# Kernel optimization log

Measured on AMD Instinct MI355X. Metric: run time of the kernel, lower is better.

Reference implementation:

```python
import jax, jax.numpy as jnp
import numpy as np

N_E = 8192
E_DIM = 64
BETA = 0.25


def setup_inputs() -> dict:
    key = jax.random.key(0)
    k_z, k_e = jax.random.split(key)
    z = jax.random.normal(k_z, (16, E_DIM, 64, 64), dtype=jnp.float32)  # b c h w
    # nn.Embedding weight init: uniform(-1/n_e, 1/n_e)
    embedding = jax.random.uniform(
        k_e, (N_E, E_DIM), dtype=jnp.float32, minval=-1.0 / N_E, maxval=1.0 / N_E
    )
    return {"z": z, "embedding": embedding}


def reference(z, embedding):
    # b c h w -> b h w c
    zc = jnp.transpose(z, (0, 2, 3, 1))
    zf = zc.reshape(-1, embedding.shape[1])  # [N, d]
    # squared euclidean distances: ||z||^2 + ||e||^2 - 2 z.e
    d = (
        jnp.sum(zf * zf, axis=1, keepdims=True)
        + jnp.sum(embedding * embedding, axis=1)
        - 2.0 * jnp.einsum("nd,kd->nk", zf, embedding)
    )  # [N, K]
    min_encoding_indices = jnp.argmin(d, axis=1)  # [N]
    z_q = jnp.take(embedding, min_encoding_indices, axis=0).reshape(zc.shape)
    # legacy=True loss
    loss = jnp.mean((jax.lax.stop_gradient(z_q) - zc) ** 2) + BETA * jnp.mean(
        (z_q - jax.lax.stop_gradient(zc)) ** 2
    )
    # straight-through estimator
    z_q = zc + jax.lax.stop_gradient(z_q - zc)
    z_q = jnp.transpose(z_q, (0, 3, 1, 2))  # b h w c -> b c h w
    return z_q, loss, min_encoding_indices
```

## Files before the change

kernel.cpp:

```cpp
#include <hip/hip_runtime.h>

#define NTOT 65536
#define KC   8192
#define DV   64
#define ZQN  4194304
#define NSPL 4
#define KSL  2048
#define NTILE 16
#define CAP2 16
#define SLA  44u
#define SLE  40u

typedef unsigned int u32;
typedef unsigned long long u64;
typedef unsigned short ushort;
typedef short short8 __attribute__((ext_vector_type(8)));
typedef float float4v __attribute__((ext_vector_type(4)));

__device__ __forceinline__ short f2bf(float x) {
    u32 u = __float_as_uint(x);
    u32 r = (u + 0x7fffu + ((u >> 16) & 1u)) >> 16;
    return (short)r;
}

__device__ __forceinline__ float exact_d(float A, float B,
                                         const float* __restrict__ zr,
                                         const float* __restrict__ e) {
#pragma clang fp contract(off)
    float u0 = 0.f, u1 = 0.f, u2 = 0.f, u3 = 0.f;
#pragma unroll
    for (int i = 0; i < 4; ++i) {
        const int t = 16 * i;
        u0 = (zr[t+0]*e[t+0]) + ((zr[t+4]*e[t+4]) + ((zr[t+8]*e[t+8]) + ((zr[t+12]*e[t+12]) + u0)));
        u1 = (zr[t+1]*e[t+1]) + ((zr[t+5]*e[t+5]) + ((zr[t+9]*e[t+9]) + ((zr[t+13]*e[t+13]) + u1)));
        u2 = (zr[t+2]*e[t+2]) + ((zr[t+6]*e[t+6]) + ((zr[t+10]*e[t+10]) + ((zr[t+14]*e[t+14]) + u2)));
        u3 = (zr[t+3]*e[t+3]) + ((zr[t+7]*e[t+7]) + ((zr[t+11]*e[t+11]) + ((zr[t+15]*e[t+15]) + u3)));
    }
    float dot = (u0 + u1) + (u2 + u3);
    return (A + B) - (2.0f * dot);
}

__global__ __launch_bounds__(256) void vq_prep(
    const float* __restrict__ emb, const float* __restrict__ z,
    float* __restrict__ nrm, float* __restrict__ An,
    u32* __restrict__ cnt, double* __restrict__ lacc,
    ushort* __restrict__ ebs) {
    const int tid = blockIdx.x * 256 + threadIdx.x;
    const int t = tid >> 10, r = tid & 1023;
    const int s = r >> 7, r2 = r & 127, h = r2 >> 6, l = r2 & 63;
    const int q = l >> 4, c = l & 15;
    const float* src = emb + (size_t)((t * 128 + s * 16 + c) * 64 + h * 32 + q * 8);
    short8 v;
#pragma unroll
    for (int j = 0; j < 8; ++j) v[j] = f2bf(src[j]);
    *reinterpret_cast<short8*>(ebs + (size_t)tid * 8) = v;
    cnt[tid] = 0u;
    {
        const float* zp = z + (size_t)(tid >> 12) * 262144 + (tid & 4095);
        double ad = 0.0;
#pragma unroll
        for (int d = 0; d < DV; ++d) {
            double x = (double)zp[(size_t)d * 4096];
            ad = fma(x, x, ad);
        }
        An[tid] = (float)ad;
    }
    if (tid < KC) {
        double sacc = 0.0;
#pragma unroll
        for (int d = 0; d < DV; ++d) {
            double x = (double)emb[(size_t)tid * DV + d];
            sacc = fma(x, x, sacc);
        }
        nrm[tid] = (float)sacc;
    }
    if (tid == 0) *lacc = 0.0;
}

__global__ __launch_bounds__(256)
void vq_pass(const float* __restrict__ z, const ushort* __restrict__ ebs,
             u32* __restrict__ cnt, u32* __restrict__ cand) {
    const int tid = threadIdx.x;
    const int lane = tid & 63;
    const int nblk = blockIdx.x & 255, ks = blockIdx.x >> 8;
    const int nb = nblk * 256 + (tid >> 6) * 64;
    const int col = lane & 15, quad = lane >> 4;
    const int nlo = nb + col;

    short8 zf[4][2];
#pragma unroll
    for (int ns = 0; ns < 4; ++ns) {
        int n = nlo + ns * 16;
        const float* zp = z + (size_t)(n >> 12) * 262144 + (n & 4095);
#pragma unroll
        for (int t2 = 0; t2 < 2; ++t2)
#pragma unroll
            for (int j = 0; j < 8; ++j)
                zf[ns][t2][j] = f2bf(zp[(size_t)(t2 * 32 + quad * 8 + j) * 4096]);
    }

    u32 r0[4] = {0, 0, 0, 0}, r1[4] = {0, 0, 0, 0}, r2[4] = {0, 0, 0, 0};
    const char* gs = (const char*)ebs + (size_t)ks * (KSL * DV * 2);

    for (int t = 0; t < NTILE; ++t) {
#pragma unroll
        for (int g2 = 0; g2 < 4; ++g2) {
            const char* tb = gs + t * 16384 + g2 * 4096;
            short8 a00 = *reinterpret_cast<const short8*>(tb + lane * 16);
            short8 a01 = *reinterpret_cast<const short8*>(tb + 1024 + lane * 16);
            short8 a10 = *reinterpret_cast<const short8*>(tb + 2048 + lane * 16);
            short8 a11 = *reinterpret_cast<const short8*>(tb + 3072 + lane * 16);
            const u32 lowc = 0x80000000u + (u32)(((t * 4 + g2) << 2) | quad);
#pragma unroll
            for (int ns = 0; ns < 4; ++ns) {
                float4v acc0 = {0.f, 0.f, 0.f, 0.f};
                float4v acc1 = {0.f, 0.f, 0.f, 0.f};
                acc0 = __builtin_amdgcn_mfma_f32_16x16x32_bf16(a00, zf[ns][0], acc0, 0, 0, 0);
                acc0 = __builtin_amdgcn_mfma_f32_16x16x32_bf16(a01, zf[ns][1], acc0, 0, 0, 0);
                acc1 = __builtin_amdgcn_mfma_f32_16x16x32_bf16(a10, zf[ns][0], acc1, 0, 0, 0);
                acc1 = __builtin_amdgcn_mfma_f32_16x16x32_bf16(a11, zf[ns][1], acc1, 0, 0, 0);
                float q0 = fmaxf(fmaxf(acc0[0], acc0[1]), acc0[2]);
                float q1 = fmaxf(fmaxf(acc0[3], acc1[0]), acc1[1]);
                float q2 = fmaxf(fmaxf(acc1[2], acc1[3]), q0);
                float m  = fmaxf(q2, q1);
                u32 e = ((u32)(int)(m * 1048576.0f) << 16) + lowc;
                u32 x  = min(r0[ns], e);
                r0[ns] = max(r0[ns], e);
                u32 y  = min(r1[ns], x);
                r1[ns] = max(r1[ns], x);
                r2[ns] = max(r2[ns], y);
            }
        }
    }

#pragma unroll
    for (int ns = 0; ns < 4; ++ns) {
        u32 m = r0[ns];
        m = max(m, __shfl_xor(m, 16));
        m = max(m, __shfl_xor(m, 32));
        const u32 thr = (m & 0xffff0000u) - (SLA << 16);
        const int n = nlo + ns * 16;
        const u32 tag = (u32)ks << 8;
        if (r0[ns] >= thr) {
            u32 p = atomicAdd(&cnt[n], 1u);
            if (p < CAP2) cand[(size_t)n * CAP2 + p] = r0[ns] | tag;
        }
        if (r1[ns] >= thr) {
            u32 p = atomicAdd(&cnt[n], 1u);
            if (p < CAP2) cand[(size_t)n * CAP2 + p] = r1[ns] | tag;
        }
        if (r2[ns] >= thr) {
            u32 p = atomicAdd(&cnt[n], 1u);
            if (p < CAP2) cand[(size_t)n * CAP2 + p] = r2[ns] | tag;
        }
    }
}

__global__ __launch_bounds__(256) void vq_e1f(
    const float* __restrict__ z, const float* __restrict__ emb,
    const float* __restrict__ nrm, const float* __restrict__ An,
    const u32* __restrict__ cnt, const u32* __restrict__ cand,
    int* __restrict__ idxw, float* __restrict__ out,
    double* __restrict__ lacc) {
    __shared__ float zs[64][40];
    __shared__ int skmin[32];
    __shared__ double red[4];
    const int tid = threadIdx.x;
    const int n0 = blockIdx.x * 32;
    const int b = n0 >> 12, hw0 = n0 & 4095;
    {
        const float* zb = z + (size_t)b * 262144 + hw0;
        const int dS = tid >> 3, i4 = (tid & 7) * 4;
#pragma unroll
        for (int j = 0; j < 2; ++j) {
            const int d = dS + 32 * j;
            float4 v = *reinterpret_cast<const float4*>(zb + (size_t)d * 4096 + i4);
            *reinterpret_cast<float4*>(&zs[d][i4]) = v;
        }
    }
    __syncthreads();

    const int li = tid >> 3;
    const int n = n0 + li;
    const int j8 = tid & 7;
    u32 c = min(cnt[n], (u32)CAP2);
    u32 emax = 0u;
    for (u32 j = 0; j < c; ++j) {
        u32 e = cand[(size_t)n * CAP2 + j];
        if (e > emax) emax = e;
    }
    const u32 ethr = (emax & 0xffff0000u) - (SLE << 16);

    float zr[DV];
#pragma unroll
    for (int d = 0; d < DV; ++d) zr[d] = zs[d][li];
    const float A = An[n];

    float dmin = 1e30f;
    int kmin = 0x7fffffff;
    const int st = j8 & 1;
    for (u32 j = (u32)(j8 >> 1); j < c; j += 4) {
        u32 e = cand[(size_t)n * CAP2 + j];
        if (e < ethr) continue;
        int s   = (int)(e >> 8) & 3;
        int grp = (int)(e >> 2) & 63;
        int q   = (int)e & 3;
        int base = s * KSL + grp * 32 + q * 4 + st * 16;
#pragma unroll
        for (int r = 0; r < 4; ++r) {
            int k = base + r;
            float d = exact_d(A, nrm[k], zr, emb + (size_t)k * DV);
            if (d < dmin || (d == dmin && k < kmin)) { dmin = d; kmin = k; }
        }
    }
    u64 key = ((u64)__float_as_uint(dmin) << 32) | (u32)kmin;
    u64 o1 = __shfl_xor(key, 1, 64); if (o1 < key) key = o1;
    u64 o2 = __shfl_xor(key, 2, 64); if (o2 < key) key = o2;
    u64 o4 = __shfl_xor(key, 4, 64); if (o4 < key) key = o4;
    if (j8 == 0) {
        int km = (int)(key & 0xffffffffu);
        idxw[n] = km;
        out[(size_t)ZQN + 1 + n] = (float)km;
        skmin[li] = km;
    }
    __syncthreads();

    const int nl = tid & 31, cg = tid >> 5;
    const int km2 = skmin[nl];
    const bool skipStore = (b >= 1 && b <= 4);
    const float4* er4 = (const float4*)(emb + (size_t)km2 * DV + cg * 8);
    float4 ev0 = er4[0], ev1 = er4[1];
    float vv[8] = {ev0.x, ev0.y, ev0.z, ev0.w, ev1.x, ev1.y, ev1.z, ev1.w};
    double lsum = 0.0;
#pragma unroll
    for (int u = 0; u < 8; ++u) {
        const int cc = cg * 8 + u;
        const float v = vv[u];
        if (!skipStore)
            out[(size_t)b * 262144 + (size_t)cc * 4096 + hw0 + nl] = v;
        double dv = (double)v - (double)zs[cc][nl];
        lsum = fma(dv, dv, lsum);
    }
#pragma unroll
    for (int off = 32; off > 0; off >>= 1)
        lsum += __shfl_down(lsum, off, 64);
    if ((tid & 63) == 0) red[tid >> 6] = lsum;
    __syncthreads();
    if (tid == 0)
        atomicAdd(lacc, red[0] + red[1] + red[2] + red[3]);
}

__global__ __launch_bounds__(256) void vq_bf(
    const float* __restrict__ emb, const int* __restrict__ idxw,
    const double* __restrict__ lacc, float* __restrict__ out) {
    const int gid = blockIdx.x * 256 + threadIdx.x;
    const int e0 = 262144 + gid * 4;
    const int b = e0 >> 18, rem = e0 & 262143;
    const int cc = rem >> 12, hw = rem & 4095;
    const int n = (b << 12) | hw;
    const int4 kk = *reinterpret_cast<const int4*>(idxw + n);
    float4 v;
    v.x = emb[(size_t)kk.x * DV + cc];
    v.y = emb[(size_t)kk.y * DV + cc];
    v.z = emb[(size_t)kk.z * DV + cc];
    v.w = emb[(size_t)kk.w * DV + cc];
    *reinterpret_cast<float4*>(out + e0) = v;
    if (gid == 0)
        out[ZQN] = (float)(1.25 * (*lacc) / (double)ZQN);
}

extern "C" void kernel_launch(void* const* d_in, const int* in_sizes, int n_in,
                              void* d_out, int out_size, void* d_ws, size_t ws_size,
                              hipStream_t stream) {
    const float* z   = (const float*)d_in[0];
    const float* emb = (const float*)d_in[1];
    float* out = (float*)d_out;

    ushort* ebs  = (ushort*)d_out;
    u32*    cand = (u32*)((char*)d_out + 1048576);
    double* lacc  = (double*)d_ws;
    float*  nrm   = (float*)((char*)d_ws + 64);
    u32*    cnt   = (u32*)((char*)d_ws + 32832);
    int*    idxw  = (int*)((char*)d_ws + 294976);
    float*  An    = (float*)((char*)d_ws + 819264);

    vq_prep<<<256, 256, 0, stream>>>(emb, z, nrm, An, cnt, lacc, ebs);
    vq_pass<<<NSPL * 256, 256, 0, stream>>>(z, ebs, cnt, cand);
    vq_e1f<<<2048, 256, 0, stream>>>(z, emb, nrm, An, cnt, cand, idxw, out, lacc);
    vq_bf<<<1024, 256, 0, stream>>>(emb, idxw, lacc, out);
}
```

Baseline: 246.4 us.

## Split exact rescoring from gather and loss, widen rescoring to 16 lanes per row

The exact-distance rescoring kernel now runs 512 threads per block with 16 lanes per row, each lane checking 2 codewords per candidate instead of 4. The gather, z_q store and loss reduction move into a separate kernel that handles all rows uniformly. That kernel computes the final loss with a last-block ticket counter, so the former final kernel is removed. The aim is more parallelism in the latency-bound rescoring step and a simpler store pattern. In exchange, z is re-read in the second kernel and there is an extra atomic ticket per block.

```diff
diff --git a/kernel.cpp b/kernel.cpp
--- a/kernel.cpp
+++ b/kernel.cpp
@@ -44,7 +44,7 @@
     const float* __restrict__ emb, const float* __restrict__ z,
     float* __restrict__ nrm, float* __restrict__ An,
     u32* __restrict__ cnt, double* __restrict__ lacc,
-    ushort* __restrict__ ebs) {
+    u32* __restrict__ ticket, ushort* __restrict__ ebs) {
     const int tid = blockIdx.x * 256 + threadIdx.x;
     const int t = tid >> 10, r = tid & 1023;
     const int s = r >> 7, r2 = r & 127, h = r2 >> 6, l = r2 & 63;
@@ -74,7 +74,7 @@
         }
         nrm[tid] = (float)sacc;
     }
-    if (tid == 0) *lacc = 0.0;
+    if (tid == 0) { *lacc = 0.0; *ticket = 0u; }
 }
 
 __global__ __launch_bounds__(256)
@@ -156,33 +156,27 @@
     }
 }
 
-__global__ __launch_bounds__(256) void vq_e1f(
+__global__ __launch_bounds__(512) void vq_e1(
     const float* __restrict__ z, const float* __restrict__ emb,
     const float* __restrict__ nrm, const float* __restrict__ An,
     const u32* __restrict__ cnt, const u32* __restrict__ cand,
-    int* __restrict__ idxw, float* __restrict__ out,
-    double* __restrict__ lacc) {
+    int* __restrict__ idxw, float* __restrict__ out) {
     __shared__ float zs[64][40];
-    __shared__ int skmin[32];
-    __shared__ double red[4];
     const int tid = threadIdx.x;
     const int n0 = blockIdx.x * 32;
     const int b = n0 >> 12, hw0 = n0 & 4095;
     {
         const float* zb = z + (size_t)b * 262144 + hw0;
         const int dS = tid >> 3, i4 = (tid & 7) * 4;
-#pragma unroll
-        for (int j = 0; j < 2; ++j) {
-            const int d = dS + 32 * j;
-            float4 v = *reinterpret_cast<const float4*>(zb + (size_t)d * 4096 + i4);
-            *reinterpret_cast<float4*>(&zs[d][i4]) = v;
-        }
+        float4 v = *reinterpret_cast<const float4*>(zb + (size_t)dS * 4096 + i4);
+        *reinterpret_cast<float4*>(&zs[dS][i4]) = v;
     }
     __syncthreads();
 
-    const int li = tid >> 3;
+    const int lane = tid & 63;
+    const int li = (tid >> 6) * 4 + (lane >> 4);
     const int n = n0 + li;
-    const int j8 = tid & 7;
+    const int j16 = lane & 15;
     u32 c = min(cnt[n], (u32)CAP2);
     u32 emax = 0u;
     for (u32 j = 0; j < c; ++j) {
@@ -198,16 +192,17 @@
 
     float dmin = 1e30f;
     int kmin = 0x7fffffff;
-    const int st = j8 & 1;
-    for (u32 j = (u32)(j8 >> 1); j < c; j += 4) {
+    const int st  = (j16 >> 1) & 1;
+    const int r0p = (j16 & 1) * 2;
+    for (u32 j = (u32)(j16 >> 2); j < c; j += 4) {
         u32 e = cand[(size_t)n * CAP2 + j];
         if (e < ethr) continue;
         int s   = (int)(e >> 8) & 3;
         int grp = (int)(e >> 2) & 63;
         int q   = (int)e & 3;
-        int base = s * KSL + grp * 32 + q * 4 + st * 16;
-#pragma unroll
-        for (int r = 0; r < 4; ++r) {
+        int base = s * KSL + grp * 32 + q * 4 + st * 16 + r0p;
+#pragma unroll
+        for (int r = 0; r < 2; ++r) {
             int k = base + r;
             float d = exact_d(A, nrm[k], zr, emb + (size_t)k * DV);
             if (d < dmin || (d == dmin && k < kmin)) { dmin = d; kmin = k; }
@@ -217,56 +212,53 @@
     u64 o1 = __shfl_xor(key, 1, 64); if (o1 < key) key = o1;
     u64 o2 = __shfl_xor(key, 2, 64); if (o2 < key) key = o2;
     u64 o4 = __shfl_xor(key, 4, 64); if (o4 < key) key = o4;
-    if (j8 == 0) {
+    u64 o8 = __shfl_xor(key, 8, 64); if (o8 < key) key = o8;
+    if (j16 == 0) {
         int km = (int)(key & 0xffffffffu);
         idxw[n] = km;
         out[(size_t)ZQN + 1 + n] = (float)km;
-        skmin[li] = km;
-    }
-    __syncthreads();
-
-    const int nl = tid & 31, cg = tid >> 5;
-    const int km2 = skmin[nl];
-    const bool skipStore = (b >= 1 && b <= 4);
-    const float4* er4 = (const float4*)(emb + (size_t)km2 * DV + cg * 8);
-    float4 ev0 = er4[0], ev1 = er4[1];
-    float vv[8] = {ev0.x, ev0.y, ev0.z, ev0.w, ev1.x, ev1.y, ev1.z, ev1.w};
+    }
+}
+
+__global__ __launch_bounds__(256) void vq_e2(
+    const float* __restrict__ z, const float* __restrict__ emb,
+    const int* __restrict__ idxw, float* __restrict__ out,
+    double* __restrict__ lacc, u32* __restrict__ ticket) {
+    __shared__ double red[4];
+    const int tid = threadIdx.x;
+    const int n = blockIdx.x * 64 + (tid & 63);
+    const int part = tid >> 6;
+    const int b = n >> 12, hw = n & 4095;
+    const int kmin = idxw[n];
+    const float* zp = z + (size_t)b * 262144 + hw;
+    const float4* er4 = (const float4*)(emb + (size_t)kmin * DV + part * 16);
     double lsum = 0.0;
 #pragma unroll
-    for (int u = 0; u < 8; ++u) {
-        const int cc = cg * 8 + u;
-        const float v = vv[u];
-        if (!skipStore)
-            out[(size_t)b * 262144 + (size_t)cc * 4096 + hw0 + nl] = v;
-        double dv = (double)v - (double)zs[cc][nl];
-        lsum = fma(dv, dv, lsum);
+    for (int i4 = 0; i4 < 4; ++i4) {
+        float4 ev = er4[i4];
+#pragma unroll
+        for (int u = 0; u < 4; ++u) {
+            int c = part * 16 + i4 * 4 + u;
+            float v = (u == 0) ? ev.x : (u == 1) ? ev.y : (u == 2) ? ev.z : ev.w;
+            out[(size_t)b * 262144 + (size_t)c * 4096 + hw] = v;
+            double dv = (double)v - (double)zp[(size_t)c * 4096];
+            lsum = fma(dv, dv, lsum);
+        }
     }
 #pragma unroll
     for (int off = 32; off > 0; off >>= 1)
         lsum += __shfl_down(lsum, off, 64);
     if ((tid & 63) == 0) red[tid >> 6] = lsum;
     __syncthreads();
-    if (tid == 0)
+    if (tid == 0) {
         atomicAdd(lacc, red[0] + red[1] + red[2] + red[3]);
-}
-
-__global__ __launch_bounds__(256) void vq_bf(
-    const float* __restrict__ emb, const int* __restrict__ idxw,
-    const double* __restrict__ lacc, float* __restrict__ out) {
-    const int gid = blockIdx.x * 256 + threadIdx.x;
-    const int e0 = 262144 + gid * 4;
-    const int b = e0 >> 18, rem = e0 & 262143;
-    const int cc = rem >> 12, hw = rem & 4095;
-    const int n = (b << 12) | hw;
-    const int4 kk = *reinterpret_cast<const int4*>(idxw + n);
-    float4 v;
-    v.x = emb[(size_t)kk.x * DV + cc];
-    v.y = emb[(size_t)kk.y * DV + cc];
-    v.z = emb[(size_t)kk.z * DV + cc];
-    v.w = emb[(size_t)kk.w * DV + cc];
-    *reinterpret_cast<float4*>(out + e0) = v;
-    if (gid == 0)
-        out[ZQN] = (float)(1.25 * (*lacc) / (double)ZQN);
+        __threadfence();
+        u32 t = atomicAdd(ticket, 1u);
+        if (t == (u32)(gridDim.x - 1)) {
+            double l = atomicAdd(lacc, 0.0);
+            out[ZQN] = (float)(1.25 * l / (double)ZQN);
+        }
+    }
 }
 
 extern "C" void kernel_launch(void* const* d_in, const int* in_sizes, int n_in,
@@ -278,14 +270,15 @@
 
     ushort* ebs  = (ushort*)d_out;
     u32*    cand = (u32*)((char*)d_out + 1048576);
-    double* lacc  = (double*)d_ws;
-    float*  nrm   = (float*)((char*)d_ws + 64);
-    u32*    cnt   = (u32*)((char*)d_ws + 32832);
-    int*    idxw  = (int*)((char*)d_ws + 294976);
-    float*  An    = (float*)((char*)d_ws + 819264);
-
-    vq_prep<<<256, 256, 0, stream>>>(emb, z, nrm, An, cnt, lacc, ebs);
+    double* lacc   = (double*)d_ws;
+    u32*    ticket = (u32*)((char*)d_ws + 8);
+    float*  nrm    = (float*)((char*)d_ws + 64);
+    u32*    cnt    = (u32*)((char*)d_ws + 32832);
+    int*    idxw   = (int*)((char*)d_ws + 294976);
+    float*  An     = (float*)((char*)d_ws + 819264);
+
+    vq_prep<<<256, 256, 0, stream>>>(emb, z, nrm, An, cnt, lacc, ticket, ebs);
     vq_pass<<<NSPL * 256, 256, 0, stream>>>(z, ebs, cnt, cand);
-    vq_e1f<<<2048, 256, 0, stream>>>(z, emb, nrm, An, cnt, cand, idxw, out, lacc);
-    vq_bf<<<1024, 256, 0, stream>>>(emb, idxw, lacc, out);
-}
+    vq_e1<<<2048, 512, 0, stream>>>(z, emb, nrm, An, cnt, cand, idxw, out);
+    vq_e2<<<1024, 256, 0, stream>>>(z, emb, idxw, out, lacc, ticket);
+}
```

After: 252.0 us. +2.3%, slower.
